# Kernel tuning notes

Hardware: AMD Instinct MI355X
Metric: run time of the kernel (lower is better)

The kernel has to match this reference:

```python
import jax, jax.numpy as jnp
import numpy as np

D = 1024
H = 16
DH = D // H
B = 8
T = 1024
EPS = 1e-5


def setup_inputs() -> dict:
    key = jax.random.key(0)
    ks = jax.random.split(key, 12)
    s = 0.02
    return {
        "x": jax.random.normal(ks[0], (B, T, D), dtype=jnp.float32),
        "ln1_scale": jnp.ones((D,), jnp.float32),
        "ln1_shift": jnp.zeros((D,), jnp.float32),
        "Wq": jax.random.normal(ks[1], (D, D), jnp.float32) * s,
        "Wk": jax.random.normal(ks[2], (D, D), jnp.float32) * s,
        "Wv": jax.random.normal(ks[3], (D, D), jnp.float32) * s,
        "Wo": jax.random.normal(ks[4], (D, D), jnp.float32) * s,
        "bo": jnp.zeros((D,), jnp.float32),
        "ln2_scale": jnp.ones((D,), jnp.float32),
        "ln2_shift": jnp.zeros((D,), jnp.float32),
        "W1": jax.random.normal(ks[5], (D, 4 * D), jnp.float32) * s,
        "b1": jnp.zeros((4 * D,), jnp.float32),
        "W2": jax.random.normal(ks[6], (4 * D, D), jnp.float32) * s,
        "b2": jnp.zeros((D,), jnp.float32),
    }


def _layernorm(x, scale, shift):
    mean = jnp.mean(x, axis=-1, keepdims=True)
    var = jnp.mean((x - mean) ** 2, axis=-1, keepdims=True)  # unbiased=False
    return (x - mean) * jax.lax.rsqrt(var + EPS) * scale + shift


def _gelu_tanh(x):
    c = jnp.sqrt(jnp.float32(2.0 / jnp.pi))
    return 0.5 * x * (1.0 + jnp.tanh(c * (x + 0.044715 * x ** 3)))


def reference(x, ln1_scale, ln1_shift, Wq, Wk, Wv, Wo, bo,
              ln2_scale, ln2_shift, W1, b1, W2, b2):
    b, t, d = x.shape
    x1 = _layernorm(x, ln1_scale, ln1_shift)
    # QKV projections (no bias), split heads -> (b, h, t, d_h)
    q = (x1 @ Wq).reshape(b, t, H, DH).transpose(0, 2, 1, 3)
    k = (x1 @ Wk).reshape(b, t, H, DH).transpose(0, 2, 1, 3)
    v = (x1 @ Wv).reshape(b, t, H, DH).transpose(0, 2, 1, 3)
    scores = jnp.einsum("bhqd,bhkd->bhqk", q, k) / jnp.sqrt(jnp.float32(DH))
    # original does tril then adds -inf upper-triangular mask -> standard causal mask
    causal = jnp.tril(jnp.ones((t, t), dtype=bool))
    scores = jnp.where(causal, scores, -jnp.inf)
    attn = jax.nn.softmax(scores, axis=-1)
    z = jnp.einsum("bhqk,bhkd->bhqd", attn, v)
    z = z.transpose(0, 2, 1, 3).reshape(b, t, d)
    x2 = z @ Wo + bo
    y = x2 + x
    y1 = _layernorm(y, ln2_scale, ln2_shift)
    y2 = _gelu_tanh(y1 @ W1 + b1) @ W2 + b2
    return y2 + y
```

## Files before the change

kernel.cpp:

```cpp
#include <hip/hip_runtime.h>

typedef unsigned short u16;
typedef __bf16 bf16x8 __attribute__((ext_vector_type(8)));
typedef float f32x4 __attribute__((ext_vector_type(4)));

#define D_MODEL 1024
#define NHEAD 16
#define DHEAD 64
#define BATCH 8
#define SEQ 1024
#define NROW 8192

__device__ __forceinline__ u16 f2bf(float f) {
  union { float f; unsigned int u; } a; a.f = f;
  unsigned int u = a.u;
  return (u16)((u + 0x7fffu + ((u >> 16) & 1u)) >> 16);
}

__device__ __forceinline__ float gelu_f(float x) {
  float x3 = x * x * x;
  return 0.5f * x * (1.0f + tanhf(0.79788456080286535588f * (x + 0.044715f * x3)));
}

__device__ __forceinline__ void async16(const void* gsrc, void* ldst) {
  __builtin_amdgcn_global_load_lds((__attribute__((address_space(1))) void*)gsrc,
                                   (__attribute__((address_space(3))) void*)ldst,
                                   16, 0, 0);
}

__global__ __launch_bounds__(256)
void wconv_kernel(const float* __restrict__ W, u16* __restrict__ WT, int K, int N) {
  __shared__ float tile[32][33];
  const int tx = threadIdx.x & 31, ty = threadIdx.x >> 5;
  const int n0 = blockIdx.x * 32, k0 = blockIdx.y * 32;
#pragma unroll
  for (int r = 0; r < 4; ++r)
    tile[ty + r * 8][tx] = W[(size_t)(k0 + ty + r * 8) * N + n0 + tx];
  __syncthreads();
#pragma unroll
  for (int r = 0; r < 4; ++r)
    WT[(size_t)(n0 + ty + r * 8) * K + k0 + tx] = f2bf(tile[tx][ty + r * 8]);
}

__global__ __launch_bounds__(256)
void ln_kernel(const float* __restrict__ x, const float* __restrict__ gamma,
               const float* __restrict__ beta, u16* __restrict__ out) {
  const int row = blockIdx.x, t = threadIdx.x;
  const float4 v = ((const float4*)(x + (size_t)row * D_MODEL))[t];
  float s  = v.x + v.y + v.z + v.w;
  float s2 = v.x * v.x + v.y * v.y + v.z * v.z + v.w * v.w;
#pragma unroll
  for (int off = 32; off >= 1; off >>= 1) {
    s  += __shfl_down(s, off);
    s2 += __shfl_down(s2, off);
  }
  __shared__ float red[8];
  const int w = t >> 6, l = t & 63;
  if (l == 0) { red[w] = s; red[4 + w] = s2; }
  __syncthreads();
  s  = red[0] + red[1] + red[2] + red[3];
  s2 = red[4] + red[5] + red[6] + red[7];
  const float mean = s * (1.0f / D_MODEL);
  const float var  = s2 * (1.0f / D_MODEL) - mean * mean;
  const float inv  = rsqrtf(var + 1e-5f);
  const float4 ga = ((const float4*)gamma)[t];
  const float4 be = ((const float4*)beta)[t];
  ushort4 ov;
  ov.x = f2bf((v.x - mean) * inv * ga.x + be.x);
  ov.y = f2bf((v.y - mean) * inv * ga.y + be.y);
  ov.z = f2bf((v.z - mean) * inv * ga.z + be.z);
  ov.w = f2bf((v.w - mean) * inv * ga.w + be.w);
  ((ushort4*)out)[(size_t)row * 256 + t] = ov;
}

#define MODE_QK 0
#define MODE_VT 1
#define MODE_F32_RES 2
#define MODE_GELU 3

template <int MODE>
__global__ __launch_bounds__(256, 2)
void gemm_bt(const u16* __restrict__ A, const u16* __restrict__ BT,
             const float* __restrict__ bias, const float* __restrict__ resid,
             void* __restrict__ outp, int M, int N, int K) {
  __shared__ u16 sA[128 * 32];
  __shared__ u16 sB[128 * 32];
  const int t = threadIdx.x;
  const int w = t >> 6, l = t & 63;
  const int c = l & 15, g = l >> 4;
  const int wr = w >> 1, wc = w & 1;
  const int bm = blockIdx.x, bn = blockIdx.y;

  f32x4 acc[4][4] = {};

  const char* Ab = (const char*)(A + (size_t)bm * 128 * K);
  const char* Bb = (const char*)(BT + (size_t)bn * 128 * K);
  const size_t ldb = (size_t)K * 2;
  const int srow = t >> 2;
  const int scolb = (t & 3) * 16;
  char* sAb = (char*)sA;
  char* sBb = (char*)sB;
  const int ldsoff = w * 1024;

  for (int k0 = 0; k0 < K; k0 += 32) {
#pragma unroll
    for (int i = 0; i < 2; ++i) {
      async16(Ab + (size_t)(srow + i * 64) * ldb + (size_t)k0 * 2 + scolb,
              sAb + i * 4096 + ldsoff);
      async16(Bb + (size_t)(srow + i * 64) * ldb + (size_t)k0 * 2 + scolb,
              sBb + i * 4096 + ldsoff);
    }
    __syncthreads();
    bf16x8 af[4], bfr[4];
#pragma unroll
    for (int m = 0; m < 4; ++m)
      af[m] = *(const bf16x8*)&sA[(wr * 64 + m * 16 + c) * 32 + g * 8];
#pragma unroll
    for (int n = 0; n < 4; ++n)
      bfr[n] = *(const bf16x8*)&sB[(wc * 64 + n * 16 + c) * 32 + g * 8];
#pragma unroll
    for (int m = 0; m < 4; ++m)
#pragma unroll
      for (int n = 0; n < 4; ++n)
        acc[m][n] = __builtin_amdgcn_mfma_f32_16x16x32_bf16(af[m], bfr[n], acc[m][n], 0, 0, 0);
    __syncthreads();
  }

#pragma unroll
  for (int m = 0; m < 4; ++m) {
    const int r0 = bm * 128 + wr * 64 + m * 16 + g * 4;
#pragma unroll
    for (int n = 0; n < 4; ++n) {
      const int cc = bn * 128 + wc * 64 + n * 16 + c;
#pragma unroll
      for (int i = 0; i < 4; ++i) {
        const int r = r0 + i;
        const float v = acc[m][n][i];
        if constexpr (MODE == MODE_QK) {
          ((u16*)outp)[(((size_t)(r >> 10) * NHEAD + (cc >> 6)) * SEQ + (r & 1023)) * DHEAD + (cc & 63)] = f2bf(v);
        } else if constexpr (MODE == MODE_VT) {
          ((u16*)outp)[(((size_t)(r >> 10) * NHEAD + (cc >> 6)) * DHEAD + (cc & 63)) * SEQ + (r & 1023)] = f2bf(v);
        } else if constexpr (MODE == MODE_F32_RES) {
          const size_t idx = (size_t)r * N + cc;
          ((float*)outp)[idx] = v + bias[cc] + resid[idx];
        } else {
          const size_t idx = (size_t)r * N + cc;
          ((u16*)outp)[idx] = f2bf(gelu_f(v + bias[cc]));
        }
      }
    }
  }
}

__global__ __launch_bounds__(256, 3)
void attn_kernel(const u16* __restrict__ q, const u16* __restrict__ k,
                 const u16* __restrict__ vT, u16* __restrict__ z) {
  __shared__ u16 sK[2][64 * 64];
  __shared__ u16 sV[2][64 * 64];
  __shared__ u16 pb[4][32 * 64];

  const int t = threadIdx.x, w = t >> 6, l = t & 63;
  const int c = l & 15, g = l >> 4;
  const int bh = blockIdx.y;
  const int qb0 = blockIdx.x * 128;
  const int qw0 = qb0 + w * 32;

  const u16* qbase = q  + (size_t)bh * SEQ * DHEAD;
  const u16* kbase = k  + (size_t)bh * SEQ * DHEAD;
  const u16* vbase = vT + (size_t)bh * DHEAD * SEQ;

  bf16x8 qf[2][2];
#pragma unroll
  for (int j = 0; j < 2; ++j)
#pragma unroll
    for (int hh = 0; hh < 2; ++hh)
      qf[j][hh] = *(const bf16x8*)&qbase[(size_t)(qw0 + j * 16 + c) * DHEAD + hh * 32 + g * 8];

  f32x4 o[4][2] = {};
  float m[2]  = {-3.0e38f, -3.0e38f};
  float ls[2] = {0.0f, 0.0f};

  const int r8 = l >> 3, ch = l & 7;
  const int sw16 = (ch ^ r8) * 16;

  auto stage = [&](int buf, int kt) {
    const int kb0 = kt * 64;
#pragma unroll
    for (int i = 0; i < 2; ++i) {
      const int row = w * 8 + i * 32 + r8;
      async16((const char*)kbase + (size_t)(kb0 + row) * 128 + sw16,
              (char*)sK[buf] + w * 1024 + i * 4096);
      async16((const char*)vbase + (size_t)row * (SEQ * 2) + (size_t)kb0 * 2 + sw16,
              (char*)sV[buf] + w * 1024 + i * 4096);
    }
  };

  const int nkt = blockIdx.x * 2 + 2;
  stage(0, 0);

  for (int kt = 0; kt < nkt; ++kt) {
    const int cur = kt & 1;
    if (kt + 1 < nkt) {
      stage(cur ^ 1, kt + 1);
      asm volatile("s_waitcnt vmcnt(4)" ::: "memory");
    } else {
      asm volatile("s_waitcnt vmcnt(0)" ::: "memory");
    }
    __builtin_amdgcn_s_barrier();

    const int kb0 = kt * 64;
    if (kb0 < qw0 + 32) {
      const u16* sKc = sK[cur];
      const u16* sVc = sV[cur];
      const int cx = c & 7;

      f32x4 st[4][2];
#pragma unroll
      for (int s = 0; s < 4; ++s) {
        const int row = s * 16 + c;
        bf16x8 kf0 = *(const bf16x8*)&sKc[row * 64 + ((0 + g) ^ cx) * 8];
        bf16x8 kf1 = *(const bf16x8*)&sKc[row * 64 + ((4 + g) ^ cx) * 8];
#pragma unroll
        for (int j = 0; j < 2; ++j) {
          f32x4 z4 = {};
          z4 = __builtin_amdgcn_mfma_f32_16x16x32_bf16(kf0, qf[j][0], z4, 0, 0, 0);
          z4 = __builtin_amdgcn_mfma_f32_16x16x32_bf16(kf1, qf[j][1], z4, 0, 0, 0);
          st[s][j] = z4;
        }
      }

      const bool full = (kb0 + 64 <= qw0 + 1);
      float tmax[2] = {-3.0e38f, -3.0e38f};
#pragma unroll
      for (int s = 0; s < 4; ++s)
#pragma unroll
        for (int j = 0; j < 2; ++j)
#pragma unroll
          for (int i = 0; i < 4; ++i) {
            float vsc = st[s][j][i] * 0.125f;
            if (!full) {
              const int key = kb0 + s * 16 + g * 4 + i;
              vsc = (key <= qw0 + j * 16 + c) ? vsc : -1.0e30f;
            }
            st[s][j][i] = vsc;
            tmax[j] = fmaxf(tmax[j], vsc);
          }
#pragma unroll
      for (int j = 0; j < 2; ++j) {
        tmax[j] = fmaxf(tmax[j], __shfl_xor(tmax[j], 16));
        tmax[j] = fmaxf(tmax[j], __shfl_xor(tmax[j], 32));
      }
      float mnew[2], sc[2], psum[2];
#pragma unroll
      for (int j = 0; j < 2; ++j) {
        mnew[j] = fmaxf(m[j], tmax[j]);
        sc[j]   = __expf(m[j] - mnew[j]);
        psum[j] = 0.0f;
      }
#pragma unroll
      for (int s = 0; s < 4; ++s)
#pragma unroll
        for (int j = 0; j < 2; ++j)
#pragma unroll
          for (int i = 0; i < 4; ++i) {
            const float pv = __expf(st[s][j][i] - mnew[j]);
            st[s][j][i] = pv;
            psum[j] += pv;
          }
#pragma unroll
      for (int j = 0; j < 2; ++j) {
        psum[j] += __shfl_xor(psum[j], 16);
        psum[j] += __shfl_xor(psum[j], 32);
        ls[j] = ls[j] * sc[j] + psum[j];
        m[j]  = mnew[j];
#pragma unroll
        for (int d = 0; d < 4; ++d) o[d][j] = o[d][j] * sc[j];
      }

      u16* pw = pb[w];
#pragma unroll
      for (int s = 0; s < 4; ++s)
#pragma unroll
        for (int j = 0; j < 2; ++j) {
          const int row = j * 16 + c;
          const int swz = (s * 2 + (g >> 1)) ^ cx;
          ushort4 pv4;
          pv4.x = f2bf(st[s][j][0]); pv4.y = f2bf(st[s][j][1]);
          pv4.z = f2bf(st[s][j][2]); pv4.w = f2bf(st[s][j][3]);
          *(ushort4*)&pw[row * 64 + swz * 8 + (g & 1) * 4] = pv4;
        }

      bf16x8 pf[2][2];
#pragma unroll
      for (int j = 0; j < 2; ++j)
#pragma unroll
        for (int ks = 0; ks < 2; ++ks)
          pf[j][ks] = *(const bf16x8*)&pw[(j * 16 + c) * 64 + ((ks * 4 + g) ^ cx) * 8];

#pragma unroll
      for (int d = 0; d < 4; ++d) {
        const int vrow = d * 16 + c;
#pragma unroll
        for (int ks = 0; ks < 2; ++ks) {
          bf16x8 vf = *(const bf16x8*)&sVc[vrow * 64 + ((ks * 4 + g) ^ cx) * 8];
#pragma unroll
          for (int j = 0; j < 2; ++j)
            o[d][j] = __builtin_amdgcn_mfma_f32_16x16x32_bf16(vf, pf[j][ks], o[d][j], 0, 0, 0);
        }
      }
    }
    __builtin_amdgcn_s_barrier();
  }

  const int b = bh >> 4, h = bh & 15;
#pragma unroll
  for (int j = 0; j < 2; ++j) {
    const float inv = 1.0f / ls[j];
    const int qrow = qw0 + j * 16 + c;
    u16* zr = z + ((size_t)b * SEQ + qrow) * D_MODEL + h * DHEAD;
#pragma unroll
    for (int d = 0; d < 4; ++d) {
      ushort4 ov;
      ov.x = f2bf(o[d][j][0] * inv); ov.y = f2bf(o[d][j][1] * inv);
      ov.z = f2bf(o[d][j][2] * inv); ov.w = f2bf(o[d][j][3] * inv);
      *(ushort4*)&zr[d * 16 + g * 4] = ov;
    }
  }
}

extern "C" void kernel_launch(void* const* d_in, const int* in_sizes, int n_in,
                              void* d_out, int out_size, void* d_ws, size_t ws_size,
                              hipStream_t stream) {
  (void)in_sizes; (void)n_in; (void)out_size; (void)ws_size;
  const float* x   = (const float*)d_in[0];
  const float* g1  = (const float*)d_in[1];
  const float* s1  = (const float*)d_in[2];
  const float* Wq  = (const float*)d_in[3];
  const float* Wk  = (const float*)d_in[4];
  const float* Wv  = (const float*)d_in[5];
  const float* Wo  = (const float*)d_in[6];
  const float* bo  = (const float*)d_in[7];
  const float* g2  = (const float*)d_in[8];
  const float* s2  = (const float*)d_in[9];
  const float* W1  = (const float*)d_in[10];
  const float* b1  = (const float*)d_in[11];
  const float* W2  = (const float*)d_in[12];
  const float* b2  = (const float*)d_in[13];
  float* out = (float*)d_out;
  char* ws = (char*)d_ws;
  const size_t MB = 1024 * 1024;

  u16* wqT = (u16*)(ws + 0 * MB);
  u16* wkT = (u16*)(ws + 2 * MB);
  u16* wvT = (u16*)(ws + 4 * MB);
  u16* woT = (u16*)(ws + 6 * MB);
  u16* w1T = (u16*)(ws + 8 * MB);
  u16* w2T = (u16*)(ws + 16 * MB);
  u16* x1  = (u16*)(ws + 24 * MB);
  u16* qb  = (u16*)(ws + 40 * MB);
  u16* kb  = (u16*)(ws + 56 * MB);
  u16* vb  = (u16*)(ws + 72 * MB);
  u16* hb  = (u16*)(ws + 24 * MB);
  u16* zb  = (u16*)(ws + 88 * MB);
  u16* y1  = (u16*)(ws + 88 * MB);
  float* yb = (float*)(ws + 104 * MB);

  wconv_kernel<<<dim3(32, 32), 256, 0, stream>>>(Wq, wqT, 1024, 1024);
  wconv_kernel<<<dim3(32, 32), 256, 0, stream>>>(Wk, wkT, 1024, 1024);
  wconv_kernel<<<dim3(32, 32), 256, 0, stream>>>(Wv, wvT, 1024, 1024);
  wconv_kernel<<<dim3(32, 32), 256, 0, stream>>>(Wo, woT, 1024, 1024);
  wconv_kernel<<<dim3(128, 32), 256, 0, stream>>>(W1, w1T, 1024, 4096);
  wconv_kernel<<<dim3(32, 128), 256, 0, stream>>>(W2, w2T, 4096, 1024);
  ln_kernel<<<NROW, 256, 0, stream>>>(x, g1, s1, x1);
  gemm_bt<MODE_QK><<<dim3(64, 8), 256, 0, stream>>>(x1, wqT, nullptr, nullptr, qb, NROW, 1024, 1024);
  gemm_bt<MODE_QK><<<dim3(64, 8), 256, 0, stream>>>(x1, wkT, nullptr, nullptr, kb, NROW, 1024, 1024);
  gemm_bt<MODE_VT><<<dim3(64, 8), 256, 0, stream>>>(x1, wvT, nullptr, nullptr, vb, NROW, 1024, 1024);
  attn_kernel<<<dim3(8, 128), 256, 0, stream>>>(qb, kb, vb, zb);
  gemm_bt<MODE_F32_RES><<<dim3(64, 8), 256, 0, stream>>>(zb, woT, bo, x, yb, NROW, 1024, 1024);
  ln_kernel<<<NROW, 256, 0, stream>>>(yb, g2, s2, y1);
  gemm_bt<MODE_GELU><<<dim3(64, 32), 256, 0, stream>>>(y1, w1T, b1, nullptr, hb, NROW, 4096, 1024);
  gemm_bt<MODE_F32_RES><<<dim3(64, 8), 256, 0, stream>>>(hb, w2T, b2, yb, out, NROW, 1024, 4096);
}
```

Before: 414.6 us.

## Double-buffer GEMM LDS tiles and use exp-based GELU

The GEMM main loop now uses two LDS buffers. The async global-to-LDS load for the next K tile is issued before the MFMAs on the current tile, with an explicit vmcnt wait and barrier at the end of each iteration, so load latency overlaps compute. GELU's tanh is rewritten as x/(1+exp(-2y)) using the fast __expf intrinsic, which is cheaper in the GELU epilogue. LDS usage doubles, which could affect the two-blocks-per-CU occupancy target, and the fast exp carries slight accuracy and overflow-edge risk.

Result: faster. 404.2 us (-2.5%).

```diff
diff --git a/kernel.cpp b/kernel.cpp
--- a/kernel.cpp
+++ b/kernel.cpp
@@ -18,8 +18,8 @@
 }
 
 __device__ __forceinline__ float gelu_f(float x) {
-  float x3 = x * x * x;
-  return 0.5f * x * (1.0f + tanhf(0.79788456080286535588f * (x + 0.044715f * x3)));
+  float y = 0.79788456080286535588f * (x + 0.044715f * x * x * x);
+  return x / (1.0f + __expf(-2.0f * y));
 }
 
 __device__ __forceinline__ void async16(const void* gsrc, void* ldst) {
@@ -83,8 +83,8 @@
 void gemm_bt(const u16* __restrict__ A, const u16* __restrict__ BT,
              const float* __restrict__ bias, const float* __restrict__ resid,
              void* __restrict__ outp, int M, int N, int K) {
-  __shared__ u16 sA[128 * 32];
-  __shared__ u16 sB[128 * 32];
+  __shared__ u16 sA[2][128 * 32];
+  __shared__ u16 sB[2][128 * 32];
   const int t = threadIdx.x;
   const int w = t >> 6, l = t & 63;
   const int c = l & 15, g = l >> 4;
@@ -98,32 +98,40 @@
   const size_t ldb = (size_t)K * 2;
   const int srow = t >> 2;
   const int scolb = (t & 3) * 16;
-  char* sAb = (char*)sA;
-  char* sBb = (char*)sB;
   const int ldsoff = w * 1024;
 
-  for (int k0 = 0; k0 < K; k0 += 32) {
+  auto stage = [&](int buf, int k0) {
 #pragma unroll
     for (int i = 0; i < 2; ++i) {
       async16(Ab + (size_t)(srow + i * 64) * ldb + (size_t)k0 * 2 + scolb,
-              sAb + i * 4096 + ldsoff);
+              (char*)sA[buf] + i * 4096 + ldsoff);
       async16(Bb + (size_t)(srow + i * 64) * ldb + (size_t)k0 * 2 + scolb,
-              sBb + i * 4096 + ldsoff);
-    }
-    __syncthreads();
+              (char*)sB[buf] + i * 4096 + ldsoff);
+    }
+  };
+
+  stage(0, 0);
+  asm volatile("s_waitcnt vmcnt(0)" ::: "memory");
+  __builtin_amdgcn_s_barrier();
+
+  const int nt = K >> 5;
+  for (int it = 0; it < nt; ++it) {
+    const int cur = it & 1;
+    if (it + 1 < nt) stage(cur ^ 1, (it + 1) << 5);
     bf16x8 af[4], bfr[4];
 #pragma unroll
     for (int m = 0; m < 4; ++m)
-      af[m] = *(const bf16x8*)&sA[(wr * 64 + m * 16 + c) * 32 + g * 8];
+      af[m] = *(const bf16x8*)&sA[cur][(wr * 64 + m * 16 + c) * 32 + g * 8];
 #pragma unroll
     for (int n = 0; n < 4; ++n)
-      bfr[n] = *(const bf16x8*)&sB[(wc * 64 + n * 16 + c) * 32 + g * 8];
+      bfr[n] = *(const bf16x8*)&sB[cur][(wc * 64 + n * 16 + c) * 32 + g * 8];
 #pragma unroll
     for (int m = 0; m < 4; ++m)
 #pragma unroll
       for (int n = 0; n < 4; ++n)
         acc[m][n] = __builtin_amdgcn_mfma_f32_16x16x32_bf16(af[m], bfr[n], acc[m][n], 0, 0, 0);
-    __syncthreads();
+    asm volatile("s_waitcnt vmcnt(0)" ::: "memory");
+    __builtin_amdgcn_s_barrier();
   }
 
 #pragma unroll
```
